# Optimization experiments

Measured on AMD Instinct MI355X. Metric: run time of the kernel, lower is better.

Reference implementation:

```python
import jax, jax.numpy as jnp
import numpy as np

CENTER_LR = 0.5  # default center_lr in _compute_centroids_mb


def setup_inputs() -> dict:
    key = jax.random.key(0)
    k1, k2, k3 = jax.random.split(key, 3)
    N, D, K = 16384, 1024, 1024
    embedded = jax.random.normal(k1, (N, D), dtype=jnp.float32)
    centers = jax.random.normal(k2, (K, D), dtype=jnp.float32)
    count = jax.random.randint(k3, (K,), 0, 10000, dtype=jnp.int32)
    return {"embedded": embedded, "centers": centers, "count": count}


def _sq_euclidean(x, c):
    # ||x - c||^2 via expansion; avoids materializing [N, K, D]
    x2 = jnp.sum(x * x, axis=1, keepdims=True)        # [N, 1]
    c2 = jnp.sum(c * c, axis=1)[None, :]              # [1, K]
    d = x2 + c2 - 2.0 * (x @ c.T)                     # [N, K]
    return jnp.maximum(d, 0.0)


def reference(embedded, centers, count):
    N, D = embedded.shape
    K = centers.shape[0]
    # predict_hard: argmin of squared euclidean distance
    dist = _sq_euclidean(embedded, centers)           # [N, K]
    labels = jnp.argmin(dist, axis=1)                 # [N]
    # _int_to_one_hot assignment matrix
    A = jax.nn.one_hot(labels, K, dtype=embedded.dtype)  # [N, K]
    # segmented reduction: batch_cluster_sums[k] = sum_{i: label_i=k} embedded[i]
    # (embedded is detached in the original -> stop_gradient)
    batch_cluster_sums = jnp.einsum('nk,nd->kd', A, jax.lax.stop_gradient(embedded))  # [K, D]
    mask_sum = jnp.sum(A, axis=0)                     # [K]
    nonzero = mask_sum != 0                           # [K]
    # count EMA (only for clusters present in the batch)
    cc = count.astype(jnp.float32)
    cc_new = jnp.where(nonzero, (1.0 - CENTER_LR) * cc + CENTER_LR * mask_sum, cc)
    per_center_lr = 1.0 / (cc_new + 1.0)              # [K]
    batch_centers = batch_cluster_sums / jnp.where(nonzero, mask_sum, 1.0)[:, None]
    new_centers = jnp.where(
        nonzero[:, None],
        (1.0 - per_center_lr)[:, None] * centers + per_center_lr[:, None] * batch_centers,
        centers,
    )
    return new_centers
```

## Files before the change

kernel.cpp:

```cpp
#include <hip/hip_runtime.h>

typedef __attribute__((ext_vector_type(8))) short bf16x8;
typedef __attribute__((ext_vector_type(4))) float f32x4;

__device__ __forceinline__ unsigned short f2bf(float f) {
    unsigned u = __float_as_uint(f);
    unsigned r = (u + 0x7FFFu + ((u >> 16) & 1u)) >> 16;
    return (unsigned short)r;
}

__device__ __forceinline__ void gload16(const unsigned short* g, unsigned short* l) {
    __builtin_amdgcn_global_load_lds((const __attribute__((address_space(1))) void*)g,
                                     (__attribute__((address_space(3))) void*)l, 16, 0, 0);
}


__global__ void conv_x_kernel(const float* __restrict__ x, unsigned short* __restrict__ xb, int total8) {
    int i = blockIdx.x * blockDim.x + threadIdx.x;
    if (i >= total8) return;
    const float4* xv = (const float4*)x;
    float4 a = xv[(size_t)i * 2];
    float4 b = xv[(size_t)i * 2 + 1];
    uint4 o;
    o.x = (unsigned)f2bf(a.x) | ((unsigned)f2bf(a.y) << 16);
    o.y = (unsigned)f2bf(a.z) | ((unsigned)f2bf(a.w) << 16);
    o.z = (unsigned)f2bf(b.x) | ((unsigned)f2bf(b.y) << 16);
    o.w = (unsigned)f2bf(b.z) | ((unsigned)f2bf(b.w) << 16);
    ((uint4*)xb)[i] = o;
}

__global__ void conv_c_kernel(const float* __restrict__ c, unsigned short* __restrict__ cb,
                              float* __restrict__ c2, int D) {
    int k = blockIdx.x;
    int tid = threadIdx.x;
    const float4 v = ((const float4*)(c + (long)k * D))[tid];
    uint2 o;
    o.x = (unsigned)f2bf(v.x) | ((unsigned)f2bf(v.y) << 16);
    o.y = (unsigned)f2bf(v.z) | ((unsigned)f2bf(v.w) << 16);
    ((uint2*)(cb + (long)k * D))[tid] = o;
    float s = v.x * v.x + v.y * v.y + v.z * v.z + v.w * v.w;
    #pragma unroll
    for (int d = 1; d < 64; d <<= 1) s += __shfl_xor(s, d, 64);
    __shared__ float wsum[4];
    int lane = tid & 63, w = tid >> 6;
    if (lane == 0) wsum[w] = s;
    __syncthreads();
    if (tid == 0) c2[k] = wsum[0] + wsum[1] + wsum[2] + wsum[3];
}

__global__ void init_packed_kernel(unsigned long long* __restrict__ p, int n) {
    int i = blockIdx.x * blockDim.x + threadIdx.x;
    if (i < n) p[i] = ~0ull;
}

__global__ void gemm_argmin_kernel(const unsigned short* __restrict__ Xb,
                                   const unsigned short* __restrict__ Cb,
                                   const float* __restrict__ c2,
                                   unsigned long long* __restrict__ packed,
                                   int D) {
    __shared__ unsigned short As[128 * 32];
    __shared__ unsigned short Bs[128 * 32];
    const int tid  = threadIdx.x;
    const int lane = tid & 63;
    const int w    = tid >> 6;
    const int wr   = w >> 1, wc = w & 1;
    const long rowbase = (long)blockIdx.x * 128;
    const int  colbase = blockIdx.y * 128;

    const int srow = tid >> 2;
    const int sq   = (tid & 3) ^ ((tid >> 2) & 3) ^ ((tid >> 4) & 3);
    const int scol = sq * 8;
    const unsigned short* ga0 = Xb + (rowbase + srow) * D + scol;
    const unsigned short* ga1 = Xb + (rowbase + 64 + srow) * D + scol;
    const unsigned short* gb0 = Cb + ((long)colbase + srow) * D + scol;
    const unsigned short* gb1 = Cb + ((long)colbase + 64 + srow) * D + scol;
    unsigned short* lA0 = &As[w * 512];
    unsigned short* lA1 = &As[2048 + w * 512];
    unsigned short* lB0 = &Bs[w * 512];
    unsigned short* lB1 = &Bs[2048 + w * 512];

    const int fr    = lane & 15;
    const int fq    = (lane >> 4) ^ (lane & 3) ^ ((lane & 12) >> 2);
    const int koffe = fq * 8;

    f32x4 acc[4][4] = {};

    for (int k0 = 0; k0 < D; k0 += 32) {
        gload16(ga0 + k0, lA0);
        gload16(ga1 + k0, lA1);
        gload16(gb0 + k0, lB0);
        gload16(gb1 + k0, lB1);
        __syncthreads();
        bf16x8 af[4], bfr[4];
        #pragma unroll
        for (int m = 0; m < 4; ++m)
            af[m] = *(const bf16x8*)&As[(wr * 64 + m * 16 + fr) * 32 + koffe];
        #pragma unroll
        for (int n = 0; n < 4; ++n)
            bfr[n] = *(const bf16x8*)&Bs[(wc * 64 + n * 16 + fr) * 32 + koffe];
        #pragma unroll
        for (int m = 0; m < 4; ++m)
            #pragma unroll
            for (int n = 0; n < 4; ++n)
                acc[m][n] = __builtin_amdgcn_mfma_f32_16x16x32_bf16(af[m], bfr[n], acc[m][n], 0, 0, 0);
        __syncthreads();
    }

    float c2v[4];
    int   kcol[4];
    #pragma unroll
    for (int n = 0; n < 4; ++n) {
        kcol[n] = colbase + wc * 64 + n * 16 + fr;
        c2v[n]  = c2[kcol[n]];
    }
    #pragma unroll
    for (int m = 0; m < 4; ++m) {
        #pragma unroll
        for (int reg = 0; reg < 4; ++reg) {
            unsigned long long best = ~0ull;
            #pragma unroll
            for (int n = 0; n < 4; ++n) {
                float score = c2v[n] - 2.0f * acc[m][n][reg];
                unsigned u = __float_as_uint(score);
                u ^= (u >> 31) ? 0xFFFFFFFFu : 0x80000000u;
                unsigned long long cand = ((unsigned long long)u << 32) | (unsigned)kcol[n];
                best = cand < best ? cand : best;
            }
            #pragma unroll
            for (int s = 1; s < 16; s <<= 1) {
                unsigned long long other = __shfl_xor(best, s, 64);
                best = other < best ? other : best;
            }
            if ((lane & 15) == 0) {
                long row = rowbase + wr * 64 + m * 16 + ((lane >> 4) << 2) + reg;
                atomicMin(&packed[row], best);
            }
        }
    }
}

__global__ void extract_labels_kernel(const unsigned long long* __restrict__ p,
                                      unsigned* __restrict__ lab, int n) {
    int i = blockIdx.x * blockDim.x + threadIdx.x;
    if (i < n) lab[i] = (unsigned)(p[i] & 0xFFFFFFFFull);
}

__global__ void segsum_partial_kernel(const unsigned* __restrict__ labels,
                                      const float* __restrict__ emb,
                                      float* __restrict__ partial,
                                      int* __restrict__ pcount,
                                      int N, int D) {
    const int k   = blockIdx.x;
    const int s   = blockIdx.y;
    const int tid = threadIdx.x;
    const int grp = tid >> 8;
    const int ct  = tid & 255;
    const int lane = tid & 63, w = tid >> 6;

    __shared__ int idxbuf[4096];
    __shared__ int cnts[16];
    __shared__ float4 red[4][256];

    const int slice = N >> 2;
    const int base0 = s * slice;
    int total = 0;
    for (int base = base0; base < base0 + slice; base += 1024) {
        const int n = base + tid;
        const bool m = (labels[n] == (unsigned)k);
        const unsigned long long bal = __ballot(m);
        if (lane == 0) cnts[w] = (int)__popcll(bal);
        __syncthreads();
        int myoff = total, run = total;
        #pragma unroll
        for (int w2 = 0; w2 < 16; ++w2) {
            if (w2 == w) myoff = run;
            run += cnts[w2];
        }
        if (m) idxbuf[myoff + (int)__popcll(bal & ((1ull << lane) - 1ull))] = n;
        total = run;
        __syncthreads();
    }

    float4 acc = {0.f, 0.f, 0.f, 0.f};
    for (int j = grp; j < total; j += 4) {
        const int row = idxbuf[j];
        const float4 v = *(const float4*)(emb + (long)row * D + ct * 4);
        acc.x += v.x; acc.y += v.y; acc.z += v.z; acc.w += v.w;
    }
    red[grp][ct] = acc;
    __syncthreads();
    if (grp == 0) {
        float4 r = red[0][ct];
        #pragma unroll
        for (int g = 1; g < 4; ++g) {
            const float4 q = red[g][ct];
            r.x += q.x; r.y += q.y; r.z += q.z; r.w += q.w;
        }
        *(float4*)(partial + ((long)(k * 4 + s)) * D + ct * 4) = r;
    }
    if (tid == 0) pcount[k * 4 + s] = total;
}

__global__ void finalize_kernel(const float* __restrict__ partial,
                                const int* __restrict__ pcount,
                                const float* __restrict__ centers,
                                const int* __restrict__ cnt,
                                float* __restrict__ out, int D) {
    const int k = blockIdx.x;
    const int ct = threadIdx.x;
    float4 acc = {0.f, 0.f, 0.f, 0.f};
    int mtot = 0;
    #pragma unroll
    for (int s = 0; s < 4; ++s) {
        const float4 p = *(const float4*)(partial + ((long)(k * 4 + s)) * D + ct * 4);
        acc.x += p.x; acc.y += p.y; acc.z += p.z; acc.w += p.w;
        mtot += pcount[k * 4 + s];
    }
    const float4 cv = *(const float4*)(centers + (long)k * D + ct * 4);
    float4 o;
    if (mtot > 0) {
        float ccn = 0.5f * (float)cnt[k] + 0.5f * (float)mtot;
        float lr  = 1.0f / (ccn + 1.0f);
        float im  = 1.0f / (float)mtot;
        float om  = 1.0f - lr;
        o.x = om * cv.x + lr * (acc.x * im);
        o.y = om * cv.y + lr * (acc.y * im);
        o.z = om * cv.z + lr * (acc.z * im);
        o.w = om * cv.w + lr * (acc.w * im);
    } else {
        o = cv;
    }
    *(float4*)(out + (long)k * D + ct * 4) = o;
}


extern "C" void kernel_launch(void* const* d_in, const int* in_sizes, int n_in,
                              void* d_out, int out_size, void* d_ws, size_t ws_size,
                              hipStream_t stream) {
    const float* emb = (const float*)d_in[0];
    const float* cen = (const float*)d_in[1];
    const int*   cnt = (const int*)d_in[2];
    float* out = (float*)d_out;
    const int K = in_sizes[2];
    const int D = in_sizes[1] / K;
    const int N = in_sizes[0] / D;

    char* ws = (char*)d_ws;
    size_t xb_bytes = (size_t)N * D * 2;
    size_t cb_bytes = (size_t)K * D * 2;
    unsigned short* Xb = (unsigned short*)ws;
    unsigned short* Cb = (unsigned short*)(ws + xb_bytes);
    float* c2 = (float*)(ws + xb_bytes + cb_bytes);
    unsigned long long* packed = (unsigned long long*)(ws + xb_bytes + cb_bytes + (size_t)K * 4);
    unsigned* labels = (unsigned*)(ws + xb_bytes + cb_bytes + (size_t)K * 4 + (size_t)N * 8);
    float* partial = (float*)ws;
    int* pcount = (int*)(ws + (size_t)K * 4 * D * 4);

    int total8 = N * D / 8;
    conv_x_kernel<<<dim3((total8 + 255) / 256), dim3(256), 0, stream>>>(emb, Xb, total8);
    conv_c_kernel<<<dim3(K), dim3(256), 0, stream>>>(cen, Cb, c2, D);
    init_packed_kernel<<<dim3((N + 255) / 256), dim3(256), 0, stream>>>(packed, N);
    gemm_argmin_kernel<<<dim3(N / 128, K / 128), dim3(256), 0, stream>>>(Xb, Cb, c2, packed, D);
    extract_labels_kernel<<<dim3((N + 255) / 256), dim3(256), 0, stream>>>(packed, labels, N);
    segsum_partial_kernel<<<dim3(K, 4), dim3(1024), 0, stream>>>(labels, emb, partial, pcount, N, D);
    finalize_kernel<<<dim3(K), dim3(256), 0, stream>>>(partial, pcount, cen, cnt, out, D);
}
```

Before: 106.6 us.

## Rework GEMM-argmin into 256x256 double-buffered pipeline and drop label extraction

```diff
diff --git a/kernel.cpp b/kernel.cpp
--- a/kernel.cpp
+++ b/kernel.cpp
@@ -13,6 +13,9 @@
     __builtin_amdgcn_global_load_lds((const __attribute__((address_space(1))) void*)g,
                                      (__attribute__((address_space(3))) void*)l, 16, 0, 0);
 }
+
+#define SCHED0() __builtin_amdgcn_sched_barrier(0)
+#define BAR2()   do { SCHED0(); __builtin_amdgcn_s_barrier(); SCHED0(); } while (0)
 
 
 __global__ void conv_x_kernel(const float* __restrict__ x, unsigned short* __restrict__ xb, int total8) {
@@ -53,57 +56,140 @@
     if (i < n) p[i] = ~0ull;
 }
 
-__global__ void gemm_argmin_kernel(const unsigned short* __restrict__ Xb,
-                                   const unsigned short* __restrict__ Cb,
-                                   const float* __restrict__ c2,
-                                   unsigned long long* __restrict__ packed,
-                                   int D) {
-    __shared__ unsigned short As[128 * 32];
-    __shared__ unsigned short Bs[128 * 32];
+__global__ void __launch_bounds__(512, 2)
+gemm_argmin_kernel(const unsigned short* __restrict__ Xb,
+                   const unsigned short* __restrict__ Cb,
+                   const float* __restrict__ c2,
+                   unsigned long long* __restrict__ packed,
+                   int D, int nt) {
+    __shared__ unsigned short sh[65536];
     const int tid  = threadIdx.x;
     const int lane = tid & 63;
     const int w    = tid >> 6;
-    const int wr   = w >> 1, wc = w & 1;
-    const long rowbase = (long)blockIdx.x * 128;
-    const int  colbase = blockIdx.y * 128;
-
-    const int srow = tid >> 2;
-    const int sq   = (tid & 3) ^ ((tid >> 2) & 3) ^ ((tid >> 4) & 3);
-    const int scol = sq * 8;
-    const unsigned short* ga0 = Xb + (rowbase + srow) * D + scol;
-    const unsigned short* ga1 = Xb + (rowbase + 64 + srow) * D + scol;
-    const unsigned short* gb0 = Cb + ((long)colbase + srow) * D + scol;
-    const unsigned short* gb1 = Cb + ((long)colbase + 64 + srow) * D + scol;
-    unsigned short* lA0 = &As[w * 512];
-    unsigned short* lA1 = &As[2048 + w * 512];
-    unsigned short* lB0 = &Bs[w * 512];
-    unsigned short* lB1 = &Bs[2048 + w * 512];
-
-    const int fr    = lane & 15;
-    const int fq    = (lane >> 4) ^ (lane & 3) ^ ((lane & 12) >> 2);
-    const int koffe = fq * 8;
-
-    f32x4 acc[4][4] = {};
-
-    for (int k0 = 0; k0 < D; k0 += 32) {
-        gload16(ga0 + k0, lA0);
-        gload16(ga1 + k0, lA1);
-        gload16(gb0 + k0, lB0);
-        gload16(gb1 + k0, lB1);
-        __syncthreads();
-        bf16x8 af[4], bfr[4];
+    const int wr   = w >> 2;
+    const int wc   = w & 3;
+    const long rowbase = (long)blockIdx.x * 256;
+    const int  colbase = blockIdx.y * 256;
+
+    const int fr = lane & 15;
+    const int g  = lane >> 4;
+    const int f7 = fr & 7;
+    const int q0 = g ^ f7;
+    const int q1 = (4 + g) ^ f7;
+    const int abase0 = (wr * 128 + fr) * 64;
+    const int bbase0 = 32768 + (wc * 64 + fr) * 64;
+
+    f32x4 acc[8][4] = {};
+    bf16x8 a[4][2], b[4][2];
+
+    auto stageA = [&](int kt, int buf) {
+        unsigned short* base = sh + buf * 16384;
+        const unsigned short* gsrc = Xb + rowbase * D + kt * 64;
+        #pragma unroll
+        for (int j = 0; j < 4; ++j) {
+            int c = j * 512 + w * 64 + lane;
+            int r = c >> 3;
+            int q = (c & 7) ^ (r & 7);
+            gload16(gsrc + (long)r * D + q * 8, base + (j * 512 + w * 64) * 8);
+        }
+    };
+    auto stageB = [&](int kt, int buf) {
+        unsigned short* base = sh + 32768 + buf * 16384;
+        const unsigned short* gsrc = Cb + (long)colbase * D + kt * 64;
+        #pragma unroll
+        for (int j = 0; j < 4; ++j) {
+            int c = j * 512 + w * 64 + lane;
+            int r = c >> 3;
+            int q = (c & 7) ^ (r & 7);
+            gload16(gsrc + (long)r * D + q * 8, base + (j * 512 + w * 64) * 8);
+        }
+    };
+
+    stageA(0, 0);
+    stageB(0, 0);
+    if (nt > 1) stageA(1, 1);
+    asm volatile("s_waitcnt vmcnt(4)" ::: "memory");
+    BAR2();
+
+    for (int t = 0; t < nt; ++t) {
+        const int buf = t & 1;
+        const int ab = abase0 + buf * 16384;
+        const int bb = bbase0 + buf * 16384;
+
+        #pragma unroll
+        for (int m = 0; m < 4; ++m) {
+            a[m][0] = *(const bf16x8*)&sh[ab + m * 1024 + q0 * 8];
+            a[m][1] = *(const bf16x8*)&sh[ab + m * 1024 + q1 * 8];
+        }
+        #pragma unroll
+        for (int n = 0; n < 2; ++n) {
+            b[n][0] = *(const bf16x8*)&sh[bb + n * 1024 + q0 * 8];
+            b[n][1] = *(const bf16x8*)&sh[bb + n * 1024 + q1 * 8];
+        }
+        if (t < nt - 1) stageB(t + 1, buf ^ 1);
+        BAR2();
+        __builtin_amdgcn_s_setprio(1);
         #pragma unroll
         for (int m = 0; m < 4; ++m)
-            af[m] = *(const bf16x8*)&As[(wr * 64 + m * 16 + fr) * 32 + koffe];
-        #pragma unroll
-        for (int n = 0; n < 4; ++n)
-            bfr[n] = *(const bf16x8*)&Bs[(wc * 64 + n * 16 + fr) * 32 + koffe];
+            #pragma unroll
+            for (int n = 0; n < 2; ++n) {
+                acc[m][n] = __builtin_amdgcn_mfma_f32_16x16x32_bf16(a[m][0], b[n][0], acc[m][n], 0, 0, 0);
+                acc[m][n] = __builtin_amdgcn_mfma_f32_16x16x32_bf16(a[m][1], b[n][1], acc[m][n], 0, 0, 0);
+            }
+        __builtin_amdgcn_s_setprio(0);
+        BAR2();
+
+        #pragma unroll
+        for (int n = 2; n < 4; ++n) {
+            b[n][0] = *(const bf16x8*)&sh[bb + n * 1024 + q0 * 8];
+            b[n][1] = *(const bf16x8*)&sh[bb + n * 1024 + q1 * 8];
+        }
+        BAR2();
+        __builtin_amdgcn_s_setprio(1);
         #pragma unroll
         for (int m = 0; m < 4; ++m)
             #pragma unroll
-            for (int n = 0; n < 4; ++n)
-                acc[m][n] = __builtin_amdgcn_mfma_f32_16x16x32_bf16(af[m], bfr[n], acc[m][n], 0, 0, 0);
-        __syncthreads();
+            for (int n = 2; n < 4; ++n) {
+                acc[m][n] = __builtin_amdgcn_mfma_f32_16x16x32_bf16(a[m][0], b[n][0], acc[m][n], 0, 0, 0);
+                acc[m][n] = __builtin_amdgcn_mfma_f32_16x16x32_bf16(a[m][1], b[n][1], acc[m][n], 0, 0, 0);
+            }
+        __builtin_amdgcn_s_setprio(0);
+        BAR2();
+
+        #pragma unroll
+        for (int m = 0; m < 4; ++m) {
+            a[m][0] = *(const bf16x8*)&sh[ab + (m + 4) * 1024 + q0 * 8];
+            a[m][1] = *(const bf16x8*)&sh[ab + (m + 4) * 1024 + q1 * 8];
+        }
+        BAR2();
+        __builtin_amdgcn_s_setprio(1);
+        #pragma unroll
+        for (int m = 0; m < 4; ++m)
+            #pragma unroll
+            for (int n = 0; n < 2; ++n) {
+                acc[m + 4][n] = __builtin_amdgcn_mfma_f32_16x16x32_bf16(a[m][0], b[n][0], acc[m + 4][n], 0, 0, 0);
+                acc[m + 4][n] = __builtin_amdgcn_mfma_f32_16x16x32_bf16(a[m][1], b[n][1], acc[m + 4][n], 0, 0, 0);
+            }
+        __builtin_amdgcn_s_setprio(0);
+        BAR2();
+
+        if (t < nt - 2) {
+            stageA(t + 2, buf);
+            asm volatile("s_waitcnt vmcnt(4)" ::: "memory");
+        } else if (t == nt - 2) {
+            asm volatile("s_waitcnt vmcnt(0)" ::: "memory");
+        }
+        BAR2();
+        __builtin_amdgcn_s_setprio(1);
+        #pragma unroll
+        for (int m = 0; m < 4; ++m)
+            #pragma unroll
+            for (int n = 2; n < 4; ++n) {
+                acc[m + 4][n] = __builtin_amdgcn_mfma_f32_16x16x32_bf16(a[m][0], b[n][0], acc[m + 4][n], 0, 0, 0);
+                acc[m + 4][n] = __builtin_amdgcn_mfma_f32_16x16x32_bf16(a[m][1], b[n][1], acc[m + 4][n], 0, 0, 0);
+            }
+        __builtin_amdgcn_s_setprio(0);
+        BAR2();
     }
 
     float c2v[4];
@@ -114,7 +200,7 @@
         c2v[n]  = c2[kcol[n]];
     }
     #pragma unroll
-    for (int m = 0; m < 4; ++m) {
+    for (int m = 0; m < 8; ++m) {
         #pragma unroll
         for (int reg = 0; reg < 4; ++reg) {
             unsigned long long best = ~0ull;
@@ -131,21 +217,15 @@
                 unsigned long long other = __shfl_xor(best, s, 64);
                 best = other < best ? other : best;
             }
-            if ((lane & 15) == 0) {
-                long row = rowbase + wr * 64 + m * 16 + ((lane >> 4) << 2) + reg;
+            if (fr == 0) {
+                long row = rowbase + wr * 128 + m * 16 + g * 4 + reg;
                 atomicMin(&packed[row], best);
             }
         }
     }
 }
 
-__global__ void extract_labels_kernel(const unsigned long long* __restrict__ p,
-                                      unsigned* __restrict__ lab, int n) {
-    int i = blockIdx.x * blockDim.x + threadIdx.x;
-    if (i < n) lab[i] = (unsigned)(p[i] & 0xFFFFFFFFull);
-}
-
-__global__ void segsum_partial_kernel(const unsigned* __restrict__ labels,
+__global__ void segsum_partial_kernel(const unsigned long long* __restrict__ packed,
                                       const float* __restrict__ emb,
                                       float* __restrict__ partial,
                                       int* __restrict__ pcount,
@@ -157,16 +237,16 @@
     const int ct  = tid & 255;
     const int lane = tid & 63, w = tid >> 6;
 
-    __shared__ int idxbuf[4096];
+    __shared__ int idxbuf[2048];
     __shared__ int cnts[16];
     __shared__ float4 red[4][256];
 
-    const int slice = N >> 2;
+    const int slice = N >> 3;
     const int base0 = s * slice;
     int total = 0;
     for (int base = base0; base < base0 + slice; base += 1024) {
         const int n = base + tid;
-        const bool m = (labels[n] == (unsigned)k);
+        const bool m = ((unsigned)(packed[n] & 0xFFFFFFFFull) == (unsigned)k);
         const unsigned long long bal = __ballot(m);
         if (lane == 0) cnts[w] = (int)__popcll(bal);
         __syncthreads();
@@ -192,13 +272,13 @@
     if (grp == 0) {
         float4 r = red[0][ct];
         #pragma unroll
-        for (int g = 1; g < 4; ++g) {
-            const float4 q = red[g][ct];
-            r.x += q.x; r.y += q.y; r.z += q.z; r.w += q.w;
-        }
-        *(float4*)(partial + ((long)(k * 4 + s)) * D + ct * 4) = r;
-    }
-    if (tid == 0) pcount[k * 4 + s] = total;
+        for (int q = 1; q < 4; ++q) {
+            const float4 v = red[q][ct];
+            r.x += v.x; r.y += v.y; r.z += v.z; r.w += v.w;
+        }
+        *(float4*)(partial + ((long)(k * 8 + s)) * D + ct * 4) = r;
+    }
+    if (tid == 0) pcount[k * 8 + s] = total;
 }
 
 __global__ void finalize_kernel(const float* __restrict__ partial,
@@ -211,10 +291,10 @@
     float4 acc = {0.f, 0.f, 0.f, 0.f};
     int mtot = 0;
     #pragma unroll
-    for (int s = 0; s < 4; ++s) {
-        const float4 p = *(const float4*)(partial + ((long)(k * 4 + s)) * D + ct * 4);
+    for (int s = 0; s < 8; ++s) {
+        const float4 p = *(const float4*)(partial + ((long)(k * 8 + s)) * D + ct * 4);
         acc.x += p.x; acc.y += p.y; acc.z += p.z; acc.w += p.w;
-        mtot += pcount[k * 4 + s];
+        mtot += pcount[k * 8 + s];
     }
     const float4 cv = *(const float4*)(centers + (long)k * D + ct * 4);
     float4 o;
@@ -252,16 +332,14 @@
     unsigned short* Cb = (unsigned short*)(ws + xb_bytes);
     float* c2 = (float*)(ws + xb_bytes + cb_bytes);
     unsigned long long* packed = (unsigned long long*)(ws + xb_bytes + cb_bytes + (size_t)K * 4);
-    unsigned* labels = (unsigned*)(ws + xb_bytes + cb_bytes + (size_t)K * 4 + (size_t)N * 8);
     float* partial = (float*)ws;
-    int* pcount = (int*)(ws + (size_t)K * 4 * D * 4);
+    int* pcount = (int*)(ws + xb_bytes + cb_bytes + (size_t)K * 4 + (size_t)N * 8);
 
     int total8 = N * D / 8;
     conv_x_kernel<<<dim3((total8 + 255) / 256), dim3(256), 0, stream>>>(emb, Xb, total8);
     conv_c_kernel<<<dim3(K), dim3(256), 0, stream>>>(cen, Cb, c2, D);
     init_packed_kernel<<<dim3((N + 255) / 256), dim3(256), 0, stream>>>(packed, N);
-    gemm_argmin_kernel<<<dim3(N / 128, K / 128), dim3(256), 0, stream>>>(Xb, Cb, c2, packed, D);
-    extract_labels_kernel<<<dim3((N + 255) / 256), dim3(256), 0, stream>>>(packed, labels, N);
-    segsum_partial_kernel<<<dim3(K, 4), dim3(1024), 0, stream>>>(labels, emb, partial, pcount, N, D);
+    gemm_argmin_kernel<<<dim3(N / 256, K / 256), dim3(512), 0, stream>>>(Xb, Cb, c2, packed, D, D / 64);
+    segsum_partial_kernel<<<dim3(K, 8), dim3(1024), 0, stream>>>(packed, emb, partial, pcount, N, D);
     finalize_kernel<<<dim3(K), dim3(256), 0, stream>>>(partial, pcount, cen, cnt, out, D);
 }
```

After: 107.0 us. No clear change (+0.3%).
